# Kernel optimization log

Measured on AMD Instinct MI355X. Metric: run time of the kernel, lower is better.

## Reference

```python
import jax, jax.numpy as jnp
import numpy as np

NUM_CLASSES = 100
SLOTS_PER_CLASS = 1
NUM_SLOTS = NUM_CLASSES * SLOTS_PER_CLASS
DIM = 512
ITERS = 3
LOSS_STATUS = 1.0
POWER = 1


def setup_inputs() -> dict:
    key = jax.random.key(0)
    ks = jax.random.split(key, 10)
    b, n, d = 128, 1024, DIM
    s = 0.02
    return {
        "inputs": jax.random.normal(ks[0], (b, n, d), jnp.float32),
        "inputs_x": jax.random.normal(ks[1], (b, n, d), jnp.float32),
        "slots_mu": jax.random.normal(ks[2], (1, 1, d), jnp.float32),
        "slots_sigma": jax.random.normal(ks[3], (1, 1, d), jnp.float32),
        "to_q_w": jax.random.normal(ks[4], (d, d), jnp.float32) * s,
        "to_q_b": jnp.zeros((d,), jnp.float32),
        "to_k_w": jax.random.normal(ks[5], (d, d), jnp.float32) * s,
        "to_k_b": jnp.zeros((d,), jnp.float32),
        "w_ih": jax.random.normal(ks[6], (3 * d, d), jnp.float32) * s,
        "w_hh": jax.random.normal(ks[7], (3 * d, d), jnp.float32) * s,
        "b_ih": jnp.zeros((3 * d,), jnp.float32),
        "b_hh": jnp.zeros((3 * d,), jnp.float32),
    }


def _gru_cell(x, h, w_ih, w_hh, b_ih, b_hh):
    # x, h: [B, d]; PyTorch nn.GRU single-step equations
    gi = x @ w_ih.T + b_ih  # [B, 3d]
    gh = h @ w_hh.T + b_hh
    ir, iz, in_ = jnp.split(gi, 3, axis=-1)
    hr, hz, hn = jnp.split(gh, 3, axis=-1)
    r = jax.nn.sigmoid(ir + hr)
    z = jax.nn.sigmoid(iz + hz)
    nnew = jnp.tanh(in_ + r * hn)
    return (1.0 - z) * nnew + z * h


def reference(inputs, inputs_x, slots_mu, slots_sigma, to_q_w, to_q_b,
              to_k_w, to_k_b, w_ih, w_hh, b_ih, b_hh):
    b, n, d = inputs.shape
    scale = d ** (-0.5)
    # slots ~ Normal(mu, |sigma|) (reparameterized)
    noise = jax.random.normal(jax.random.key(1), (b, NUM_SLOTS, d), inputs.dtype)
    slots = slots_mu + jnp.abs(slots_sigma) * noise
    k = inputs @ to_k_w.T + to_k_b  # [b, n, d]
    attn = None
    updates = None
    for _ in range(ITERS):
        slots_prev = slots
        q = slots @ to_q_w.T + to_q_b  # [b, S, d]
        dots = jnp.einsum('bid,bjd->bij', q, k) * scale  # [b, S, n]
        attn = jax.nn.softmax(dots, axis=-1)
        updates = jnp.einsum('bjd,bij->bid', inputs_x, attn) / d  # [b, S, d]
        h = _gru_cell(updates.reshape(-1, d), slots_prev.reshape(-1, d),
                      w_ih, w_hh, b_ih, b_hh)
        slots = h.reshape(b, NUM_SLOTS, d)
    # slots_per_class == 1: no class aggregation needed
    slot_loss = jnp.sum(jax.nn.relu(attn)) / (b * NUM_SLOTS * n)
    out = LOSS_STATUS * jnp.sum(updates, axis=2)  # [b, NUM_SLOTS]
    return out, slot_loss ** POWER
```

## Files before the change

### kernel.cpp

```cpp
#include <hip/hip_runtime.h>
#include <math.h>

typedef __attribute__((ext_vector_type(4))) float f32x4;
typedef __attribute__((ext_vector_type(8))) short s16x8;

__device__ __forceinline__ unsigned rotl32(unsigned x, int r) {
    return (x << r) | (x >> (32 - r));
}
__device__ __forceinline__ unsigned short f2bf(float x) {
    unsigned u = __float_as_uint(x);
    unsigned r = (u + 0x7FFFu + ((u >> 16) & 1u)) >> 16;
    return (unsigned short)r;
}
__device__ __forceinline__ float b2f(unsigned short b) {
    return __uint_as_float((unsigned)b << 16);
}
__device__ __forceinline__ void async16(const unsigned short* g, unsigned short* l) {
    __builtin_amdgcn_global_load_lds(
        (const __attribute__((address_space(1))) void*)g,
        (__attribute__((address_space(3))) void*)l, 16, 0, 0);
}

__device__ __forceinline__ float bits_to_normal(unsigned bits) {
    float f = __uint_as_float((bits >> 9) | 0x3F800000u) - 1.0f;
    const float lo = -0.99999994f;
    float u = f * 2.0f + lo;
    u = fmaxf(lo, u);
    float w = -log1pf(-u * u);
    float p;
    if (w < 5.0f) {
        w -= 2.5f;
        p = 2.81022636e-08f;
        p = fmaf(p, w, 3.43273939e-07f);
        p = fmaf(p, w, -3.5233877e-06f);
        p = fmaf(p, w, -4.39150654e-06f);
        p = fmaf(p, w, 0.00021858087f);
        p = fmaf(p, w, -0.00125372503f);
        p = fmaf(p, w, -0.00417768164f);
        p = fmaf(p, w, 0.246640727f);
        p = fmaf(p, w, 1.50140941f);
    } else {
        w = sqrtf(w) - 3.0f;
        p = -0.000200214257f;
        p = fmaf(p, w, 0.000100950558f);
        p = fmaf(p, w, 0.00134934322f);
        p = fmaf(p, w, -0.00367342844f);
        p = fmaf(p, w, 0.00573950773f);
        p = fmaf(p, w, -0.0076224613f);
        p = fmaf(p, w, 0.00943887047f);
        p = fmaf(p, w, 1.00167406f);
        p = fmaf(p, w, 2.83297682f);
    }
    return 1.41421356237f * (p * u);
}

__global__ __launch_bounds__(256)
void k_init_slots(const float* __restrict__ mu, const float* __restrict__ sigma,
                  float* __restrict__ slots, unsigned short* __restrict__ slotsb) {
    unsigned e = blockIdx.x * 256u + threadIdx.x;
    const unsigned ks0 = 0u, ks1 = 1u, ks2 = 0x1BD11BDBu;
    unsigned x0 = 0u + ks0;
    unsigned x1 = e + ks1;
#define TF_RND(r) { x0 += x1; x1 = rotl32(x1, r); x1 ^= x0; }
    TF_RND(13) TF_RND(15) TF_RND(26) TF_RND(6)   x0 += ks1; x1 += ks2 + 1u;
    TF_RND(17) TF_RND(29) TF_RND(16) TF_RND(24)  x0 += ks2; x1 += ks0 + 2u;
    TF_RND(13) TF_RND(15) TF_RND(26) TF_RND(6)   x0 += ks0; x1 += ks1 + 3u;
    TF_RND(17) TF_RND(29) TF_RND(16) TF_RND(24)  x0 += ks1; x1 += ks2 + 4u;
    TF_RND(13) TF_RND(15) TF_RND(26) TF_RND(6)   x0 += ks2; x1 += ks0 + 5u;
#undef TF_RND
    unsigned bits = x0 ^ x1;
    int d0 = (int)(e & 511u);
    float v = mu[d0] + fabsf(sigma[d0]) * bits_to_normal(bits);
    slots[e] = v;
    slotsb[e] = f2bf(v);
}

__global__ __launch_bounds__(256)
void k_cast(const float* __restrict__ s, unsigned short* __restrict__ d, int n4) {
    int i = blockIdx.x * 256 + threadIdx.x;
    if (i < n4) {
        float4 v = ((const float4*)s)[i];
        ((ushort4*)d)[i] = make_ushort4(f2bf(v.x), f2bf(v.y), f2bf(v.z), f2bf(v.w));
    }
}

__global__ __launch_bounds__(256)
void k_transpose_cast(const float* __restrict__ x, unsigned short* __restrict__ xT) {
    __shared__ float t[32][33];
    int b = blockIdx.z;
    int j0 = blockIdx.x * 32;
    int d0 = blockIdx.y * 32;
    int tx = threadIdx.x & 31, ty = threadIdx.x >> 5;
    const float* xp = x + ((long long)b * 1024 + j0) * 512 + d0;
#pragma unroll
    for (int q = 0; q < 4; q++) {
        int j = ty + q * 8;
        t[j][tx] = xp[(long long)j * 512 + tx];
    }
    __syncthreads();
    unsigned short* op = xT + ((long long)b * 512 + d0) * 1024 + j0;
#pragma unroll
    for (int q = 0; q < 4; q++) {
        int d = ty + q * 8;
        op[(long long)d * 1024 + tx] = f2bf(t[tx][d]);
    }
}

template<bool A_F32, bool HAS_BIAS, bool XSWZ = false>
__global__ __launch_bounds__(256)
void k_mfma_nt(const void* __restrict__ Araw, long long sA,
               const unsigned short* __restrict__ B, long long sB,
               unsigned short* __restrict__ C, long long sC,
               const float* __restrict__ bias,
               int M, int N, int K, float alpha) {
    __shared__ __align__(16) unsigned short As[128 * 32];
    __shared__ __align__(16) unsigned short Bs[128 * 32];
    const int tid = threadIdx.x;
    const unsigned short* Ab = (const unsigned short*)Araw + (long long)blockIdx.z * sA;
    const float* Af = (const float*)Araw + (long long)blockIdx.z * sA;
    const unsigned short* Bb = B + (long long)blockIdx.z * sB;
    C += (long long)blockIdx.z * sC;

    int nb, mb;
    if (XSWZ) {
        unsigned L = blockIdx.x;
        unsigned x = L & 7u;
        unsigned j = L >> 3u;
        unsigned panels = gridDim.x >> 5u;
        mb = (int)(x * panels + (j >> 2u));
        nb = (int)(j & 3u);
    } else {
        nb = blockIdx.x;
        mb = blockIdx.y;
    }
    const int n0 = nb * 128;
    const int m0 = mb * 128;

    const int lane = tid & 63;
    const int wave = tid >> 6;
    const int wm = (wave >> 1) * 64;
    const int wn = (wave & 1) * 64;
    const int lrow = lane & 15;
    const int lquad = lane >> 4;

    f32x4 acc[4][4];
#pragma unroll
    for (int i = 0; i < 4; i++)
#pragma unroll
        for (int j = 0; j < 4; j++) acc[i][j] = (f32x4)0.0f;

    const int arow_s = tid >> 1;
    const int akh_s = (tid & 1) * 16;
    int arowg_s = m0 + arow_s; if (arowg_s >= M) arowg_s = M - 1;

    for (int k0 = 0; k0 < K; k0 += 32) {
        float4 f0, f1, f2, f3;
        if (A_F32) {
            const float* ap = Af + (long long)arowg_s * K + k0 + akh_s;
            f0 = *(const float4*)(ap);
            f1 = *(const float4*)(ap + 4);
            f2 = *(const float4*)(ap + 8);
            f3 = *(const float4*)(ap + 12);
        }
        __syncthreads();
        if (A_F32) {
            s16x8 p0, p1;
            p0[0] = (short)f2bf(f0.x); p0[1] = (short)f2bf(f0.y);
            p0[2] = (short)f2bf(f0.z); p0[3] = (short)f2bf(f0.w);
            p0[4] = (short)f2bf(f1.x); p0[5] = (short)f2bf(f1.y);
            p0[6] = (short)f2bf(f1.z); p0[7] = (short)f2bf(f1.w);
            p1[0] = (short)f2bf(f2.x); p1[1] = (short)f2bf(f2.y);
            p1[2] = (short)f2bf(f2.z); p1[3] = (short)f2bf(f2.w);
            p1[4] = (short)f2bf(f3.x); p1[5] = (short)f2bf(f3.y);
            p1[6] = (short)f2bf(f3.z); p1[7] = (short)f2bf(f3.w);
            *(s16x8*)&As[arow_s * 32 + akh_s] = p0;
            *(s16x8*)&As[arow_s * 32 + akh_s + 8] = p1;
        } else {
#pragma unroll
            for (int p = 0; p < 2; p++) {
                int c = p * 256 + tid;
                int row = c >> 2;
                int kc = (c & 3) * 8;
                int rowg = m0 + row; if (rowg >= M) rowg = M - 1;
                async16(Ab + (long long)rowg * K + k0 + kc,
                        &As[(p * 256 + (tid & ~63)) * 8]);
            }
        }
#pragma unroll
        for (int p = 0; p < 2; p++) {
            int c = p * 256 + tid;
            int row = c >> 2;
            int kc = (c & 3) * 8;
            async16(Bb + (long long)(n0 + row) * K + k0 + kc,
                    &Bs[(p * 256 + (tid & ~63)) * 8]);
        }
        __syncthreads();

        s16x8 afr[4], bfr[4];
#pragma unroll
        for (int i = 0; i < 4; i++)
            afr[i] = *(const s16x8*)&As[(wm + i * 16 + lrow) * 32 + lquad * 8];
#pragma unroll
        for (int j = 0; j < 4; j++)
            bfr[j] = *(const s16x8*)&Bs[(wn + j * 16 + lrow) * 32 + lquad * 8];
#pragma unroll
        for (int i = 0; i < 4; i++)
#pragma unroll
            for (int j = 0; j < 4; j++)
                acc[i][j] = __builtin_amdgcn_mfma_f32_16x16x32_bf16(
                    afr[i], bfr[j], acc[i][j], 0, 0, 0);
    }

#pragma unroll
    for (int i = 0; i < 4; i++) {
#pragma unroll
        for (int r = 0; r < 4; r++) {
            int grow = m0 + wm + i * 16 + lquad * 4 + r;
            if (grow < M) {
#pragma unroll
                for (int j = 0; j < 4; j++) {
                    int gcol = n0 + wn + j * 16 + lrow;
                    float v = acc[i][j][r] * alpha;
                    if (HAS_BIAS) v += bias[gcol];
                    C[(long long)grow * N + gcol] = f2bf(v);
                }
            }
        }
    }
}

__global__ __launch_bounds__(256)
void k_softmax_bf(unsigned short* __restrict__ attn) {
    __shared__ float red[8];
    unsigned short* p = attn + (long long)blockIdx.x * 1024;
    ushort4 v = ((const ushort4*)p)[threadIdx.x];
    float a0 = b2f(v.x), a1 = b2f(v.y), a2 = b2f(v.z), a3 = b2f(v.w);
    float mx = fmaxf(fmaxf(a0, a1), fmaxf(a2, a3));
#pragma unroll
    for (int off = 32; off; off >>= 1) mx = fmaxf(mx, __shfl_down(mx, off));
    int wid = threadIdx.x >> 6, lane = threadIdx.x & 63;
    if (lane == 0) red[wid] = mx;
    __syncthreads();
    mx = fmaxf(fmaxf(red[0], red[1]), fmaxf(red[2], red[3]));
    float e0 = expf(a0 - mx), e1 = expf(a1 - mx);
    float e2 = expf(a2 - mx), e3 = expf(a3 - mx);
    float s = (e0 + e1) + (e2 + e3);
#pragma unroll
    for (int off = 32; off; off >>= 1) s += __shfl_down(s, off);
    if (lane == 0) red[4 + wid] = s;
    __syncthreads();
    float inv = 1.0f / ((red[4] + red[5]) + (red[6] + red[7]));
    ((ushort4*)p)[threadIdx.x] =
        make_ushort4(f2bf(e0 * inv), f2bf(e1 * inv), f2bf(e2 * inv), f2bf(e3 * inv));
}

__global__ __launch_bounds__(256)
void k_gru_pw(const unsigned short* __restrict__ gi, const unsigned short* __restrict__ gh,
              const float* __restrict__ bih, const float* __restrict__ bhh,
              float* __restrict__ slots, unsigned short* __restrict__ slotsb) {
    long long idx = (long long)blockIdx.x * 256 + threadIdx.x;
    int m = (int)(idx >> 9);
    int c = (int)(idx & 511);
    const unsigned short* gim = gi + (long long)m * 1536;
    const unsigned short* ghm = gh + (long long)m * 1536;
    float r = 1.0f / (1.0f + expf(-(b2f(gim[c]) + b2f(ghm[c]) + bih[c] + bhh[c])));
    float z = 1.0f / (1.0f + expf(-(b2f(gim[512 + c]) + b2f(ghm[512 + c])
                                    + bih[512 + c] + bhh[512 + c])));
    float hn = b2f(ghm[1024 + c]) + bhh[1024 + c];
    float nn = tanhf(b2f(gim[1024 + c]) + bih[1024 + c] + r * hn);
    float hp = slots[idx];
    float h = (1.0f - z) * nn + z * hp;
    slots[idx] = h;
    slotsb[idx] = f2bf(h);
}

__global__ __launch_bounds__(128)
void k_out(const unsigned short* __restrict__ updb, float* __restrict__ out) {
    __shared__ float r2[2];
    const unsigned short* p = updb + (long long)blockIdx.x * 512;
    ushort4 v = ((const ushort4*)p)[threadIdx.x];
    float s = (b2f(v.x) + b2f(v.y)) + (b2f(v.z) + b2f(v.w));
#pragma unroll
    for (int off = 32; off; off >>= 1) s += __shfl_down(s, off);
    if ((threadIdx.x & 63) == 0) r2[threadIdx.x >> 6] = s;
    __syncthreads();
    if (threadIdx.x == 0) {
        out[blockIdx.x] = r2[0] + r2[1];
        if (blockIdx.x == 0) out[12800] = 0.0009765625f;
    }
}

extern "C" void kernel_launch(void* const* d_in, const int* in_sizes, int n_in,
                              void* d_out, int out_size, void* d_ws, size_t ws_size,
                              hipStream_t stream) {
    const float* inputs   = (const float*)d_in[0];
    const float* inputs_x = (const float*)d_in[1];
    const float* mu       = (const float*)d_in[2];
    const float* sigma    = (const float*)d_in[3];
    const float* to_q_w   = (const float*)d_in[4];
    const float* to_q_b   = (const float*)d_in[5];
    const float* to_k_w   = (const float*)d_in[6];
    const float* to_k_b   = (const float*)d_in[7];
    const float* w_ih     = (const float*)d_in[8];
    const float* w_hh     = (const float*)d_in[9];
    const float* b_ih     = (const float*)d_in[10];
    const float* b_hh     = (const float*)d_in[11];
    float* out = (float*)d_out;

    char* base = (char*)d_ws;
    unsigned short* k_bf   = (unsigned short*)(base);
    unsigned short* xT     = (unsigned short*)(base + 134217728ll);
    float*          slots  = (float*)        (base + 268435456ll);
    unsigned short* slotsb = (unsigned short*)(base + 294649856ll);
    unsigned short* updb   = (unsigned short*)(base + 307757056ll);
    char* regionA          = base + 320864256ll;
    char* regionB          = base + 360185856ll;
    unsigned short* Wk_bf  = (unsigned short*)(base + 399507456ll);
    unsigned short* Wq_bf  = (unsigned short*)(base + 400031744ll);
    unsigned short* Wih_bf = (unsigned short*)(base + 400556032ll);
    unsigned short* Whh_bf = (unsigned short*)(base + 402128896ll);
    unsigned short* q_bf   = (unsigned short*)regionA;
    unsigned short* gi_bf  = (unsigned short*)regionA;
    unsigned short* attnb  = (unsigned short*)regionB;
    unsigned short* gh_bf  = (unsigned short*)regionB;

    k_init_slots<<<25600, 256, 0, stream>>>(mu, sigma, slots, slotsb);
    k_cast<<<256, 256, 0, stream>>>(to_k_w, Wk_bf, 65536);
    k_cast<<<256, 256, 0, stream>>>(to_q_w, Wq_bf, 65536);
    k_cast<<<768, 256, 0, stream>>>(w_ih, Wih_bf, 196608);
    k_cast<<<768, 256, 0, stream>>>(w_hh, Whh_bf, 196608);
    k_transpose_cast<<<dim3(32, 16, 128), 256, 0, stream>>>(inputs_x, xT);

    k_mfma_nt<true, true, true><<<dim3(4096, 1, 1), 256, 0, stream>>>(
        inputs, 0, Wk_bf, 0, k_bf, 0, to_k_b, 131072, 512, 512, 1.0f);

    const float scale = 0.044194173824159216f;
    for (int it = 0; it < 3; ++it) {
        k_mfma_nt<false, true><<<dim3(4, 100, 1), 256, 0, stream>>>(
            slotsb, 0, Wq_bf, 0, q_bf, 0, to_q_b, 12800, 512, 512, 1.0f);
        k_mfma_nt<false, false><<<dim3(8, 1, 128), 256, 0, stream>>>(
            q_bf, 51200, k_bf, 524288, attnb, 102400, nullptr, 100, 1024, 512, scale);
        k_softmax_bf<<<12800, 256, 0, stream>>>(attnb);
        k_mfma_nt<false, false><<<dim3(4, 1, 128), 256, 0, stream>>>(
            attnb, 102400, xT, 524288, updb, 51200, nullptr, 100, 512, 1024, 0.001953125f);
        k_mfma_nt<false, false><<<dim3(12, 100, 1), 256, 0, stream>>>(
            updb, 0, Wih_bf, 0, gi_bf, 0, nullptr, 12800, 1536, 512, 1.0f);
        k_mfma_nt<false, false><<<dim3(12, 100, 1), 256, 0, stream>>>(
            slotsb, 0, Whh_bf, 0, gh_bf, 0, nullptr, 12800, 1536, 512, 1.0f);
        k_gru_pw<<<25600, 256, 0, stream>>>(gi_bf, gh_bf, b_ih, b_hh, slots, slotsb);
    }
    k_out<<<12800, 128, 0, stream>>>(updb, out);
}
```

Measured before the change: 1.467 ms.

## Double-buffer LDS tiles in MFMA GEMM to overlap loads with compute

Splits the A and B shared-memory tiles into two buffers so the next K-tile is fetched while MFMAs run on the current one. This removes one barrier per iteration. For the fp32-A path, the global loads are issued early and the bf16 conversion and store happen after the MFMAs. The cost is doubled LDS use (32KB per block), which may reduce occupancy. The async loads may also be waited on at the barrier regardless, which would limit the overlap.

```diff
diff --git a/kernel.cpp b/kernel.cpp
--- a/kernel.cpp
+++ b/kernel.cpp
@@ -113,8 +113,8 @@
                unsigned short* __restrict__ C, long long sC,
                const float* __restrict__ bias,
                int M, int N, int K, float alpha) {
-    __shared__ __align__(16) unsigned short As[128 * 32];
-    __shared__ __align__(16) unsigned short Bs[128 * 32];
+    __shared__ __align__(16) unsigned short As[2][128 * 32];
+    __shared__ __align__(16) unsigned short Bs[2][128 * 32];
     const int tid = threadIdx.x;
     const unsigned short* Ab = (const unsigned short*)Araw + (long long)blockIdx.z * sA;
     const float* Af = (const float*)Araw + (long long)blockIdx.z * sA;
@@ -153,62 +153,87 @@
     const int akh_s = (tid & 1) * 16;
     int arowg_s = m0 + arow_s; if (arowg_s >= M) arowg_s = M - 1;
 
-    for (int k0 = 0; k0 < K; k0 += 32) {
-        float4 f0, f1, f2, f3;
-        if (A_F32) {
-            const float* ap = Af + (long long)arowg_s * K + k0 + akh_s;
-            f0 = *(const float4*)(ap);
-            f1 = *(const float4*)(ap + 4);
-            f2 = *(const float4*)(ap + 8);
-            f3 = *(const float4*)(ap + 12);
+    const int c0_row = tid >> 2;
+    const int c0_kc = (tid & 3) * 8;
+    const int ldsoff0 = (tid & ~63) * 8;
+    const int ldsoff1 = (256 + (tid & ~63)) * 8;
+
+    float4 f0, f1, f2, f3;
+
+    auto loadAf32 = [&](int k0) {
+        const float* ap = Af + (long long)arowg_s * K + k0 + akh_s;
+        f0 = *(const float4*)(ap);
+        f1 = *(const float4*)(ap + 4);
+        f2 = *(const float4*)(ap + 8);
+        f3 = *(const float4*)(ap + 12);
+    };
+    auto castA = [&](unsigned short* dst) {
+        s16x8 p0, p1;
+        p0[0] = (short)f2bf(f0.x); p0[1] = (short)f2bf(f0.y);
+        p0[2] = (short)f2bf(f0.z); p0[3] = (short)f2bf(f0.w);
+        p0[4] = (short)f2bf(f1.x); p0[5] = (short)f2bf(f1.y);
+        p0[6] = (short)f2bf(f1.z); p0[7] = (short)f2bf(f1.w);
+        p1[0] = (short)f2bf(f2.x); p1[1] = (short)f2bf(f2.y);
+        p1[2] = (short)f2bf(f2.z); p1[3] = (short)f2bf(f2.w);
+        p1[4] = (short)f2bf(f3.x); p1[5] = (short)f2bf(f3.y);
+        p1[6] = (short)f2bf(f3.z); p1[7] = (short)f2bf(f3.w);
+        *(s16x8*)&dst[arow_s * 32 + akh_s] = p0;
+        *(s16x8*)&dst[arow_s * 32 + akh_s + 8] = p1;
+    };
+    auto stageAasync = [&](int k0, unsigned short* dst) {
+        int r0 = m0 + c0_row;       if (r0 >= M) r0 = M - 1;
+        int r1 = m0 + 64 + c0_row;  if (r1 >= M) r1 = M - 1;
+        async16(Ab + (long long)r0 * K + k0 + c0_kc, &dst[ldsoff0]);
+        async16(Ab + (long long)r1 * K + k0 + c0_kc, &dst[ldsoff1]);
+    };
+    auto stageB = [&](int k0, unsigned short* dst) {
+        async16(Bb + (long long)(n0 + c0_row) * K + k0 + c0_kc, &dst[ldsoff0]);
+        async16(Bb + (long long)(n0 + 64 + c0_row) * K + k0 + c0_kc, &dst[ldsoff1]);
+    };
+
+    const int nt = K >> 5;
+
+    if (A_F32) {
+        loadAf32(0);
+        stageB(0, Bs[0]);
+        castA(As[0]);
+    } else {
+        stageAasync(0, As[0]);
+        stageB(0, Bs[0]);
+    }
+    __syncthreads();
+
+    int cur = 0;
+    for (int t = 0; t < nt; ++t) {
+        const int nxt = cur ^ 1;
+        const bool more = (t + 1 < nt);
+        if (more) {
+            const int k1 = (t + 1) << 5;
+            if (A_F32) {
+                loadAf32(k1);
+            } else {
+                stageAasync(k1, As[nxt]);
+            }
+            stageB(k1, Bs[nxt]);
         }
-        __syncthreads();
-        if (A_F32) {
-            s16x8 p0, p1;
-            p0[0] = (short)f2bf(f0.x); p0[1] = (short)f2bf(f0.y);
-            p0[2] = (short)f2bf(f0.z); p0[3] = (short)f2bf(f0.w);
-            p0[4] = (short)f2bf(f1.x); p0[5] = (short)f2bf(f1.y);
-            p0[6] = (short)f2bf(f1.z); p0[7] = (short)f2bf(f1.w);
-            p1[0] = (short)f2bf(f2.x); p1[1] = (short)f2bf(f2.y);
-            p1[2] = (short)f2bf(f2.z); p1[3] = (short)f2bf(f2.w);
-            p1[4] = (short)f2bf(f3.x); p1[5] = (short)f2bf(f3.y);
-            p1[6] = (short)f2bf(f3.z); p1[7] = (short)f2bf(f3.w);
-            *(s16x8*)&As[arow_s * 32 + akh_s] = p0;
-            *(s16x8*)&As[arow_s * 32 + akh_s + 8] = p1;
-        } else {
-#pragma unroll
-            for (int p = 0; p < 2; p++) {
-                int c = p * 256 + tid;
-                int row = c >> 2;
-                int kc = (c & 3) * 8;
-                int rowg = m0 + row; if (rowg >= M) rowg = M - 1;
-                async16(Ab + (long long)rowg * K + k0 + kc,
-                        &As[(p * 256 + (tid & ~63)) * 8]);
-            }
-        }
-#pragma unroll
-        for (int p = 0; p < 2; p++) {
-            int c = p * 256 + tid;
-            int row = c >> 2;
-            int kc = (c & 3) * 8;
-            async16(Bb + (long long)(n0 + row) * K + k0 + kc,
-                    &Bs[(p * 256 + (tid & ~63)) * 8]);
-        }
-        __syncthreads();
-
+        const unsigned short* Asc = As[cur];
+        const unsigned short* Bsc = Bs[cur];
         s16x8 afr[4], bfr[4];
 #pragma unroll
         for (int i = 0; i < 4; i++)
-            afr[i] = *(const s16x8*)&As[(wm + i * 16 + lrow) * 32 + lquad * 8];
+            afr[i] = *(const s16x8*)&Asc[(wm + i * 16 + lrow) * 32 + lquad * 8];
 #pragma unroll
         for (int j = 0; j < 4; j++)
-            bfr[j] = *(const s16x8*)&Bs[(wn + j * 16 + lrow) * 32 + lquad * 8];
+            bfr[j] = *(const s16x8*)&Bsc[(wn + j * 16 + lrow) * 32 + lquad * 8];
 #pragma unroll
         for (int i = 0; i < 4; i++)
 #pragma unroll
             for (int j = 0; j < 4; j++)
                 acc[i][j] = __builtin_amdgcn_mfma_f32_16x16x32_bf16(
                     afr[i], bfr[j], acc[i][j], 0, 0, 0);
+        if (more && A_F32) castA(As[nxt]);
+        __syncthreads();
+        cur = nxt;
     }
 
 #pragma unroll
```

Result: no change. 1.448 ms (-1.3%).
